# Kernel tuning notes

Measured on AMD Instinct MI355X. Metric: run time of the kernel, lower is better.

Reference implementation:

```python
import jax, jax.numpy as jnp
import numpy as np

S, HID, H, D, G = 2048, 4096, 32, 128, 2   # seq, hidden, heads, head_dim, kv groups
ROT = D // 2                               # rotary applied to first half of head_dim
QKV = HID + 2 * G * D                      # 4608


def setup_inputs() -> dict:
    key = jax.random.key(0)
    k1, k2, k3 = jax.random.split(key, 3)
    sc = 0.02
    return {
        "hidden_states": jax.random.normal(k1, (S, HID), jnp.float32),
        "W_qkv": jax.random.normal(k2, (HID, QKV), jnp.float32) * sc,
        "b_qkv": jnp.zeros((QKV,), jnp.float32),
        "W_dense": jax.random.normal(k3, (HID, HID), jnp.float32) * sc,
    }


def _rope(x, pos):
    # x: [S, n_heads, ROT]; interleaved-pair rotation (ChatGLM2 convention)
    half = ROT // 2
    inv_freq = 10000.0 ** (-jnp.arange(0, ROT, 2, dtype=jnp.float32) / ROT)  # [half]
    theta = pos[:, None] * inv_freq                                          # [S, half]
    cos = jnp.cos(theta)[:, None, :]
    sin = jnp.sin(theta)[:, None, :]
    xp = x.reshape(x.shape[0], x.shape[1], half, 2)
    x0, x1 = xp[..., 0], xp[..., 1]
    out = jnp.stack([x0 * cos - x1 * sin, x1 * cos + x0 * sin], axis=-1)
    return out.reshape(x.shape)


def reference(hidden_states, W_qkv, b_qkv, W_dense):
    qkv = hidden_states @ W_qkv + b_qkv            # [S, QKV]
    q = qkv[:, : H * D].reshape(S, H, D)           # [S, H, D]
    k = qkv[:, H * D : H * D + G * D].reshape(S, G, D)
    v = qkv[:, H * D + G * D :].reshape(S, G, D)

    pos = jnp.arange(S, dtype=jnp.float32)
    q = jnp.concatenate([_rope(q[..., :ROT], pos), q[..., ROT:]], axis=-1)
    k = jnp.concatenate([_rope(k[..., :ROT], pos), k[..., ROT:]], axis=-1)

    gidx = jnp.arange(H) % G                       # head -> kv group (MQA/GQA)
    kh = k[:, gidx, :]                             # [S, H, D]
    vh = v[:, gidx, :]

    scores = jnp.einsum('shd,thd->hst', q, kh) / jnp.sqrt(jnp.float32(D))
    causal = jnp.tril(jnp.ones((S, S), bool))
    scores = jnp.where(causal[None], scores, jnp.float32(-1e9))
    p = jax.nn.softmax(scores, axis=-1)            # [H, S, S]
    ctx = jnp.einsum('hst,thd->shd', p, vh).reshape(S, HID)
    return ctx @ W_dense
```

## Files before the change

kernel.cpp:

```cpp
#include <hip/hip_runtime.h>
#include <hip/hip_bf16.h>

#define S_LEN 2048
#define HIDN  4096
#define NH    32
#define HD    128
#define QKV_N 4608
#define K_OFF 4096
#define V_OFF 4352
#define SCALE 0.08838834764831845f

typedef __attribute__((ext_vector_type(8))) short   short8;
typedef __attribute__((ext_vector_type(4))) float   f32x4;
typedef __attribute__((ext_vector_type(4))) unsigned short ushort4v;
typedef __attribute__((ext_vector_type(8))) unsigned short ushort8;

typedef __attribute__((address_space(1))) const unsigned int GU32;
typedef __attribute__((address_space(3))) unsigned int LU32;

__device__ __forceinline__ void async16(const void* g, void* l) {
  __builtin_amdgcn_global_load_lds((GU32*)g, (LU32*)l, 16, 0, 0);
}

__device__ __forceinline__ unsigned short f2bf(float x) {
  __hip_bfloat16 h = __float2bfloat16(x);
  return *reinterpret_cast<unsigned short*>(&h);
}
__device__ __forceinline__ float bf2f(unsigned short u) {
  __hip_bfloat16 h = *reinterpret_cast<__hip_bfloat16*>(&u);
  return __bfloat162float(h);
}

__global__ void k_cvt_bf16(const float* __restrict__ in, unsigned short* __restrict__ out, int n4) {
  int i = blockIdx.x * 256 + threadIdx.x;
  if (i >= n4) return;
  const float4 v = reinterpret_cast<const float4*>(in)[i];
  ushort4v o = { f2bf(v.x), f2bf(v.y), f2bf(v.z), f2bf(v.w) };
  reinterpret_cast<ushort4v*>(out)[i] = o;
}

__global__ __launch_bounds__(256) void k_transpose_cvt(const float* __restrict__ W,
                                                       unsigned short* __restrict__ WT,
                                                       int K, int N) {
  __shared__ float tl[64][65];
  const int n0 = blockIdx.x * 64, k0 = blockIdx.y * 64;
  const int t = threadIdx.x;
  const int r = t >> 4, c4 = (t & 15) << 2;
#pragma unroll
  for (int p = 0; p < 4; ++p) {
    int krow = p * 16 + r;
    const float4 v = *reinterpret_cast<const float4*>(&W[(size_t)(k0 + krow) * N + n0 + c4]);
    tl[krow][c4 + 0] = v.x; tl[krow][c4 + 1] = v.y;
    tl[krow][c4 + 2] = v.z; tl[krow][c4 + 3] = v.w;
  }
  __syncthreads();
#pragma unroll
  for (int p = 0; p < 4; ++p) {
    int nrow = p * 16 + r;
    ushort4v o = { f2bf(tl[c4 + 0][nrow]), f2bf(tl[c4 + 1][nrow]),
                   f2bf(tl[c4 + 2][nrow]), f2bf(tl[c4 + 3][nrow]) };
    *reinterpret_cast<ushort4v*>(&WT[(size_t)(n0 + nrow) * K + k0 + c4]) = o;
  }
}

template <int BIAS, int OUTBF>
__global__ __launch_bounds__(256, 2) void k_gemm_bt(const unsigned short* __restrict__ A,
                                                    const unsigned short* __restrict__ Bt,
                                                    const float* __restrict__ bias,
                                                    void* __restrict__ Cout,
                                                    int M, int N, int K) {
  __shared__ __align__(16) unsigned char lds[32768];
  const int tid = threadIdx.x;
  const int l = tid & 63, w = tid >> 6;
  const int wr = w >> 1, wc = w & 1;
  const int l16 = l & 15, lh = l >> 4;
  const int nx = N >> 7;
  const int cpx = gridDim.x >> 3;
  const int wg = (blockIdx.x & 7) * cpx + (blockIdx.x >> 3);
  const int m0 = (wg / nx) * 128, n0 = (wg % nx) * 128;
  const size_t rowK = (size_t)K * 2;
  const char* Ab = (const char*)A + (size_t)m0 * rowK;
  const char* Bb = (const char*)Bt + (size_t)n0 * rowK;
  f32x4 acc[4][4] = {};
  const int nkt = K >> 6;
  for (int kt = 0; kt < nkt; ++kt) {
    const int kbyte = kt << 7;
#pragma unroll
    for (int rr = 0; rr < 4; ++rr) {
      int off = rr * 4096 + tid * 16;
      int row = off >> 7;
      int col = (off & 127) ^ ((row & 7) << 4);
      async16(Ab + (size_t)row * rowK + kbyte + col, lds + off);
    }
#pragma unroll
    for (int rr = 0; rr < 4; ++rr) {
      int off = rr * 4096 + tid * 16;
      int row = off >> 7;
      int col = (off & 127) ^ ((row & 7) << 4);
      async16(Bb + (size_t)row * rowK + kbyte + col, lds + 16384 + off);
    }
    __syncthreads();
#pragma unroll
    for (int kk = 0; kk < 2; ++kk) {
      short8 af[4], bfr[4];
#pragma unroll
      for (int m = 0; m < 4; ++m) {
        int arow = wr * 64 + m * 16 + l16;
        int byte = (arow << 7) + kk * 64 + lh * 16;
        byte ^= (arow & 7) << 4;
        af[m] = *reinterpret_cast<const short8*>(lds + byte);
      }
#pragma unroll
      for (int n = 0; n < 4; ++n) {
        int brow = wc * 64 + n * 16 + l16;
        int byte = (brow << 7) + kk * 64 + lh * 16;
        byte ^= (brow & 7) << 4;
        bfr[n] = *reinterpret_cast<const short8*>(lds + 16384 + byte);
      }
#pragma unroll
      for (int m = 0; m < 4; ++m)
#pragma unroll
        for (int n = 0; n < 4; ++n)
          acc[m][n] = __builtin_amdgcn_mfma_f32_16x16x32_bf16(af[m], bfr[n], acc[m][n], 0, 0, 0);
    }
    __syncthreads();
  }
#pragma unroll
  for (int m = 0; m < 4; ++m) {
    int grow = m0 + wr * 64 + m * 16 + lh * 4;
#pragma unroll
    for (int n = 0; n < 4; ++n) {
      int gcol = n0 + wc * 64 + n * 16 + l16;
      float bv = BIAS ? bias[gcol] : 0.f;
      f32x4 v = acc[m][n];
#pragma unroll
      for (int j = 0; j < 4; ++j) {
        float val = v[j] + bv;
        if (OUTBF) ((unsigned short*)Cout)[(size_t)(grow + j) * N + gcol] = f2bf(val);
        else       ((float*)Cout)[(size_t)(grow + j) * N + gcol] = val;
      }
    }
  }
}

__global__ void k_rope(unsigned short* __restrict__ qkv) {
  const int p = blockIdx.x * 64 + threadIdx.x;
  const int s = blockIdx.y;
  const int i = p & 31;
  const int hh = p >> 5;
  const int col = (hh < 32) ? (hh * HD + 2 * i) : (K_OFF + (hh - 32) * HD + 2 * i);
  unsigned int* ptr = (unsigned int*)(qkv + (size_t)s * QKV_N + col);
  unsigned int both = *ptr;
  float x0 = bf2f((unsigned short)(both & 0xffffu));
  float x1 = bf2f((unsigned short)(both >> 16));
  float inv = expf(-0.28782313662425572f * (float)i);
  float theta = (float)s * inv;
  float sn, cs;
  sincosf(theta, &sn, &cs);
  float y0 = x0 * cs - x1 * sn;
  float y1 = x1 * cs + x0 * sn;
  *ptr = (unsigned int)f2bf(y0) | ((unsigned int)f2bf(y1) << 16);
}

__global__ __launch_bounds__(256) void k_transpose_v(const unsigned short* __restrict__ qkv,
                                                     unsigned short* __restrict__ Vt) {
  __shared__ __align__(16) unsigned short tl[64][72];
  const int st = blockIdx.x * 64;
  const int dt = blockIdx.y * 64;
  const int g = blockIdx.z;
  const int t = threadIdx.x;
  const int r = t >> 3;
  const int seg = (t & 7) * 8;
#pragma unroll
  for (int p = 0; p < 2; ++p) {
    int srow = p * 32 + r;
    ushort8 v = *reinterpret_cast<const ushort8*>(
        &qkv[(size_t)(st + srow) * QKV_N + V_OFF + g * HD + dt + seg]);
    *reinterpret_cast<ushort8*>(&tl[srow][seg]) = v;
  }
  __syncthreads();
#pragma unroll
  for (int p = 0; p < 2; ++p) {
    int drow = p * 32 + r;
    ushort8 o;
#pragma unroll
    for (int i = 0; i < 8; ++i) o[i] = tl[seg + i][drow];
    *reinterpret_cast<ushort8*>(&Vt[((size_t)g * HD + dt + drow) * S_LEN + st + seg]) = o;
  }
}

__global__ __launch_bounds__(512) void k_attn(const unsigned short* __restrict__ qkv,
                                              const unsigned short* __restrict__ Vt,
                                              unsigned short* __restrict__ ctx) {
  __shared__ __align__(16) unsigned char lds[81920];
  const int tid = threadIdx.x;
  const int l = tid & 63, w = tid >> 6;
  const int l16 = l & 15, lh = l >> 4;
  const int b = blockIdx.x;
  const int h = b & 31;
  const int g = h & 1;
  const int bt = b >> 5;
  const int tier = (b < 256) ? bt : 23 - bt;
  const int q0 = (15 - tier) * 128;
  const int qw = q0 + w * 16;
  const int nkt = (q0 >> 6) + 2;

  const char* Kbase = (const char*)(qkv + K_OFF + g * HD);
  const char* Vbase = (const char*)(Vt + (size_t)g * HD * S_LEN);

  short8 vones;
#pragma unroll
  for (int e = 0; e < 8; ++e) vones[e] = (short)0x3F80;

  short8 qf[4];
#pragma unroll
  for (int ks = 0; ks < 4; ++ks)
    qf[ks] = *reinterpret_cast<const short8*>(
        qkv + (size_t)(qw + l16) * QKV_N + h * HD + ks * 32 + lh * 8);
  asm volatile("s_waitcnt vmcnt(0)" ::: "memory");

  f32x4 o[8] = {};
  f32x4 lacc = {};
  float m_run = -1e30f;

#pragma unroll
  for (int rr = 0; rr < 2; ++rr) {
    int off = rr * 8192 + tid * 16;
    int row = off >> 8;
    int col = (off & 255) ^ ((row & 7) << 4);
    async16(Kbase + (size_t)row * (QKV_N * 2) + col, lds + off);
  }
#pragma unroll
  for (int rr = 0; rr < 2; ++rr) {
    int off = rr * 8192 + tid * 16;
    int row = off >> 7;
    int col = (off & 127) ^ ((row & 7) << 4);
    async16(Vbase + (size_t)row * (S_LEN * 2) + col, lds + 32768 + off);
  }

  for (int kt = 0; kt < nkt; ++kt) {
    const int k0 = kt << 6;
    if (kt + 1 < nkt) {
      const int bsel = ((kt + 1) & 1) * 16384;
      const int kn = k0 + 64;
      __builtin_amdgcn_sched_barrier(0);
#pragma unroll
      for (int rr = 0; rr < 2; ++rr) {
        int off = rr * 8192 + tid * 16;
        int row = off >> 8;
        int col = (off & 255) ^ ((row & 7) << 4);
        async16(Kbase + (size_t)(kn + row) * (QKV_N * 2) + col, lds + bsel + off);
      }
#pragma unroll
      for (int rr = 0; rr < 2; ++rr) {
        int off = rr * 8192 + tid * 16;
        int row = off >> 7;
        int col = (off & 127) ^ ((row & 7) << 4);
        async16(Vbase + (size_t)row * (S_LEN * 2) + kn * 2 + col, lds + 32768 + bsel + off);
      }
      __builtin_amdgcn_sched_barrier(0);
      asm volatile("s_waitcnt vmcnt(4)" ::: "memory");
    } else {
      asm volatile("s_waitcnt vmcnt(0)" ::: "memory");
    }
    __builtin_amdgcn_s_barrier();
    __builtin_amdgcn_sched_barrier(0);

    const unsigned char* Kl = lds + (kt & 1) * 16384;
    const unsigned char* Vl = lds + 32768 + (kt & 1) * 16384;

    const bool active = (qw + 15 >= k0);
    if (active) {
      f32x4 sf[4] = {};
      __builtin_amdgcn_s_setprio(1);
#pragma unroll
      for (int n = 0; n < 4; ++n) {
        int krow = n * 16 + l16;
        int swz = (krow & 7) << 4;
#pragma unroll
        for (int ks = 0; ks < 4; ++ks) {
          int byte = (krow << 8) + ks * 64 + lh * 16;
          short8 kf = *reinterpret_cast<const short8*>(Kl + (byte ^ swz));
          sf[n] = __builtin_amdgcn_mfma_f32_16x16x32_bf16(qf[ks], kf, sf[n], 0, 0, 0);
        }
      }
      __builtin_amdgcn_s_setprio(0);

      const int qrow0 = qw + lh * 4;
      float tmax = -1e30f;
#pragma unroll
      for (int n = 0; n < 4; ++n) {
        int key = k0 + n * 16 + l16;
#pragma unroll
        for (int j = 0; j < 4; ++j) {
          float v = sf[n][j] * SCALE;
          v = (key <= qrow0 + j) ? v : -1e30f;
          sf[n][j] = v;
          tmax = fmaxf(tmax, v);
        }
      }
#pragma unroll
      for (int d = 1; d < 64; d <<= 1) tmax = fmaxf(tmax, __shfl_xor(tmax, d, 64));
      if (tmax > m_run + 8.f) {
        float fsc = __expf(m_run - tmax);
        m_run = tmax;
#pragma unroll
        for (int n8 = 0; n8 < 8; ++n8) o[n8] *= fsc;
        lacc *= fsc;
      }

      unsigned char* Pb = lds + 65536 + w * 2048;
#pragma unroll
      for (int n = 0; n < 4; ++n)
#pragma unroll
        for (int j = 0; j < 4; ++j) {
          int row = lh * 4 + j;
          int byte = (row << 7) + (n * 16 + l16) * 2;
          byte ^= (row & 7) << 4;
          *(unsigned short*)(Pb + byte) = f2bf(__expf(sf[n][j] - m_run));
        }

      __builtin_amdgcn_s_setprio(1);
#pragma unroll
      for (int kk = 0; kk < 2; ++kk) {
        int pbyte = (l16 << 7) + kk * 64 + lh * 16;
        pbyte ^= (l16 & 7) << 4;
        short8 pa = *reinterpret_cast<const short8*>(Pb + pbyte);
        lacc = __builtin_amdgcn_mfma_f32_16x16x32_bf16(pa, vones, lacc, 0, 0, 0);
#pragma unroll
        for (int n8 = 0; n8 < 8; ++n8) {
          int vrow = n8 * 16 + l16;
          int vbyte = (vrow << 7) + kk * 64 + lh * 16;
          vbyte ^= (vrow & 7) << 4;
          short8 vb = *reinterpret_cast<const short8*>(Vl + vbyte);
          o[n8] = __builtin_amdgcn_mfma_f32_16x16x32_bf16(pa, vb, o[n8], 0, 0, 0);
        }
      }
      __builtin_amdgcn_s_setprio(0);
    }
    __builtin_amdgcn_s_barrier();
  }

#pragma unroll
  for (int n8 = 0; n8 < 8; ++n8) {
    int col = h * HD + n8 * 16 + l16;
#pragma unroll
    for (int j = 0; j < 4; ++j) {
      int row = qw + lh * 4 + j;
      ctx[(size_t)row * HIDN + col] = f2bf(o[n8][j] / lacc[j]);
    }
  }
}

extern "C" void kernel_launch(void* const* d_in, const int* in_sizes, int n_in,
                              void* d_out, int out_size, void* d_ws, size_t ws_size,
                              hipStream_t stream) {
  const float* hidden = (const float*)d_in[0];
  const float* Wqkv = (const float*)d_in[1];
  const float* bqkv = (const float*)d_in[2];
  const float* Wd = (const float*)d_in[3];
  char* ws = (char*)d_ws;
  unsigned short* hid_bf = (unsigned short*)(ws);
  unsigned short* WqkvT  = (unsigned short*)(ws + 16777216);
  unsigned short* WdT    = (unsigned short*)(ws + 54525952);
  unsigned short* qkv    = (unsigned short*)(ws + 88080384);
  unsigned short* Vt     = (unsigned short*)(ws + 106954752);
  unsigned short* ctx    = (unsigned short*)(ws + 108003328);

  k_cvt_bf16<<<8192, 256, 0, stream>>>(hidden, hid_bf, 2097152);
  k_transpose_cvt<<<dim3(72, 64), 256, 0, stream>>>(Wqkv, WqkvT, 4096, 4608);
  k_transpose_cvt<<<dim3(64, 64), 256, 0, stream>>>(Wd, WdT, 4096, 4096);
  k_gemm_bt<1, 1><<<576, 256, 0, stream>>>(hid_bf, WqkvT, bqkv, qkv, 2048, 4608, 4096);
  k_rope<<<dim3(17, 2048), 64, 0, stream>>>(qkv);
  k_transpose_v<<<dim3(32, 2, 2), 256, 0, stream>>>(qkv, Vt);
  k_attn<<<512, 512, 0, stream>>>(qkv, Vt, ctx);
  k_gemm_bt<0, 0><<<512, 256, 0, stream>>>(ctx, WdT, nullptr, d_out, 2048, 4096, 4096);
}
```

Before: 315.8 us.

## Switch attention to 32x32x16 MFMA with 4 waves of 32 query rows

The attention kernel moves from 16x16x32 to 32x32x16 bf16 MFMA tiles, so each wave now owns 32 query rows and blocks shrink from 512 to 256 threads (4 waves). The K/V staging loop is factored into a helper that issues more loads per thread with a wider K swizzle, and the wait count is adjusted to match. The aim is fewer LDS fragment reads per FLOP and better MFMA throughput, at the cost of more accumulator registers per wave and fewer waves per block to hide latency.

```diff
diff --git a/kernel.cpp b/kernel.cpp
--- a/kernel.cpp
+++ b/kernel.cpp
@@ -12,6 +12,7 @@
 
 typedef __attribute__((ext_vector_type(8))) short   short8;
 typedef __attribute__((ext_vector_type(4))) float   f32x4;
+typedef __attribute__((ext_vector_type(16))) float  f32x16;
 typedef __attribute__((ext_vector_type(4))) unsigned short ushort4v;
 typedef __attribute__((ext_vector_type(8))) unsigned short ushort8;
 
@@ -189,20 +190,40 @@
   }
 }
 
-__global__ __launch_bounds__(512) void k_attn(const unsigned short* __restrict__ qkv,
+__device__ __forceinline__ void stage_kv2(const char* Kb, const char* Vb,
+                                          unsigned char* ldsK, unsigned char* ldsV, int tid) {
+  __builtin_amdgcn_sched_barrier(0);
+#pragma unroll
+  for (int rr = 0; rr < 4; ++rr) {
+    int off = rr * 4096 + tid * 16;
+    int row = off >> 8;
+    int col = (off & 255) ^ ((row & 15) << 4);
+    async16(Kb + (size_t)row * (QKV_N * 2) + col, ldsK + off);
+  }
+#pragma unroll
+  for (int rr = 0; rr < 4; ++rr) {
+    int off = rr * 4096 + tid * 16;
+    int row = off >> 7;
+    int col = (off & 127) ^ ((row & 7) << 4);
+    async16(Vb + (size_t)row * (S_LEN * 2) + col, ldsV + off);
+  }
+  __builtin_amdgcn_sched_barrier(0);
+}
+
+__global__ __launch_bounds__(256) void k_attn(const unsigned short* __restrict__ qkv,
                                               const unsigned short* __restrict__ Vt,
                                               unsigned short* __restrict__ ctx) {
   __shared__ __align__(16) unsigned char lds[81920];
   const int tid = threadIdx.x;
   const int l = tid & 63, w = tid >> 6;
-  const int l16 = l & 15, lh = l >> 4;
+  const int l32 = l & 31, hi = l >> 5;
   const int b = blockIdx.x;
   const int h = b & 31;
   const int g = h & 1;
   const int bt = b >> 5;
   const int tier = (b < 256) ? bt : 23 - bt;
   const int q0 = (15 - tier) * 128;
-  const int qw = q0 + w * 16;
+  const int qw = q0 + w * 32;
   const int nkt = (q0 >> 6) + 2;
 
   const char* Kbase = (const char*)(qkv + K_OFF + g * HD);
@@ -212,54 +233,26 @@
 #pragma unroll
   for (int e = 0; e < 8; ++e) vones[e] = (short)0x3F80;
 
-  short8 qf[4];
-#pragma unroll
-  for (int ks = 0; ks < 4; ++ks)
+  short8 qf[8];
+#pragma unroll
+  for (int ks = 0; ks < 8; ++ks)
     qf[ks] = *reinterpret_cast<const short8*>(
-        qkv + (size_t)(qw + l16) * QKV_N + h * HD + ks * 32 + lh * 8);
+        qkv + (size_t)(qw + l32) * QKV_N + h * HD + ks * 16 + hi * 8);
   asm volatile("s_waitcnt vmcnt(0)" ::: "memory");
 
-  f32x4 o[8] = {};
-  f32x4 lacc = {};
+  f32x16 o[4] = {};
+  f32x16 lacc = {};
   float m_run = -1e30f;
 
-#pragma unroll
-  for (int rr = 0; rr < 2; ++rr) {
-    int off = rr * 8192 + tid * 16;
-    int row = off >> 8;
-    int col = (off & 255) ^ ((row & 7) << 4);
-    async16(Kbase + (size_t)row * (QKV_N * 2) + col, lds + off);
-  }
-#pragma unroll
-  for (int rr = 0; rr < 2; ++rr) {
-    int off = rr * 8192 + tid * 16;
-    int row = off >> 7;
-    int col = (off & 127) ^ ((row & 7) << 4);
-    async16(Vbase + (size_t)row * (S_LEN * 2) + col, lds + 32768 + off);
-  }
+  stage_kv2(Kbase, Vbase, lds, lds + 32768, tid);
 
   for (int kt = 0; kt < nkt; ++kt) {
     const int k0 = kt << 6;
     if (kt + 1 < nkt) {
       const int bsel = ((kt + 1) & 1) * 16384;
-      const int kn = k0 + 64;
-      __builtin_amdgcn_sched_barrier(0);
-#pragma unroll
-      for (int rr = 0; rr < 2; ++rr) {
-        int off = rr * 8192 + tid * 16;
-        int row = off >> 8;
-        int col = (off & 255) ^ ((row & 7) << 4);
-        async16(Kbase + (size_t)(kn + row) * (QKV_N * 2) + col, lds + bsel + off);
-      }
-#pragma unroll
-      for (int rr = 0; rr < 2; ++rr) {
-        int off = rr * 8192 + tid * 16;
-        int row = off >> 7;
-        int col = (off & 127) ^ ((row & 7) << 4);
-        async16(Vbase + (size_t)row * (S_LEN * 2) + kn * 2 + col, lds + 32768 + bsel + off);
-      }
-      __builtin_amdgcn_sched_barrier(0);
-      asm volatile("s_waitcnt vmcnt(4)" ::: "memory");
+      stage_kv2(Kbase + (size_t)(k0 + 64) * (QKV_N * 2), Vbase + (size_t)(k0 + 64) * 2,
+                lds + bsel, lds + 32768 + bsel, tid);
+      asm volatile("s_waitcnt vmcnt(8)" ::: "memory");
     } else {
       asm volatile("s_waitcnt vmcnt(0)" ::: "memory");
     }
@@ -269,33 +262,32 @@
     const unsigned char* Kl = lds + (kt & 1) * 16384;
     const unsigned char* Vl = lds + 32768 + (kt & 1) * 16384;
 
-    const bool active = (qw + 15 >= k0);
+    const bool active = (qw + 31 >= k0);
     if (active) {
-      f32x4 sf[4] = {};
+      f32x16 sf[2] = {};
       __builtin_amdgcn_s_setprio(1);
 #pragma unroll
-      for (int n = 0; n < 4; ++n) {
-        int krow = n * 16 + l16;
-        int swz = (krow & 7) << 4;
-#pragma unroll
-        for (int ks = 0; ks < 4; ++ks) {
-          int byte = (krow << 8) + ks * 64 + lh * 16;
-          short8 kf = *reinterpret_cast<const short8*>(Kl + (byte ^ swz));
-          sf[n] = __builtin_amdgcn_mfma_f32_16x16x32_bf16(qf[ks], kf, sf[n], 0, 0, 0);
+      for (int ks = 0; ks < 8; ++ks)
+#pragma unroll
+        for (int kb = 0; kb < 2; ++kb) {
+          int krow = kb * 32 + l32;
+          int byte = krow * 256 + ks * 32 + hi * 16;
+          byte ^= (krow & 15) << 4;
+          short8 kf = *reinterpret_cast<const short8*>(Kl + byte);
+          sf[kb] = __builtin_amdgcn_mfma_f32_32x32x16_bf16(qf[ks], kf, sf[kb], 0, 0, 0);
         }
-      }
       __builtin_amdgcn_s_setprio(0);
 
-      const int qrow0 = qw + lh * 4;
       float tmax = -1e30f;
 #pragma unroll
-      for (int n = 0; n < 4; ++n) {
-        int key = k0 + n * 16 + l16;
-#pragma unroll
-        for (int j = 0; j < 4; ++j) {
-          float v = sf[n][j] * SCALE;
-          v = (key <= qrow0 + j) ? v : -1e30f;
-          sf[n][j] = v;
+      for (int kb = 0; kb < 2; ++kb) {
+        int key = k0 + kb * 32 + l32;
+#pragma unroll
+        for (int r = 0; r < 16; ++r) {
+          int qrow = qw + (r & 3) + 8 * (r >> 2) + 4 * hi;
+          float v = sf[kb][r] * SCALE;
+          v = (key <= qrow) ? v : -1e30f;
+          sf[kb][r] = v;
           tmax = fmaxf(tmax, v);
         }
       }
@@ -305,35 +297,35 @@
         float fsc = __expf(m_run - tmax);
         m_run = tmax;
 #pragma unroll
-        for (int n8 = 0; n8 < 8; ++n8) o[n8] *= fsc;
+        for (int nf = 0; nf < 4; ++nf) o[nf] *= fsc;
         lacc *= fsc;
       }
 
-      unsigned char* Pb = lds + 65536 + w * 2048;
-#pragma unroll
-      for (int n = 0; n < 4; ++n)
-#pragma unroll
-        for (int j = 0; j < 4; ++j) {
-          int row = lh * 4 + j;
-          int byte = (row << 7) + (n * 16 + l16) * 2;
+      unsigned char* Pw = lds + 65536 + w * 4096;
+#pragma unroll
+      for (int kb = 0; kb < 2; ++kb)
+#pragma unroll
+        for (int r = 0; r < 16; ++r) {
+          int row = (r & 3) + 8 * (r >> 2) + 4 * hi;
+          int byte = row * 128 + (kb * 32 + l32) * 2;
           byte ^= (row & 7) << 4;
-          *(unsigned short*)(Pb + byte) = f2bf(__expf(sf[n][j] - m_run));
+          *(unsigned short*)(Pw + byte) = f2bf(__expf(sf[kb][r] - m_run));
         }
 
       __builtin_amdgcn_s_setprio(1);
 #pragma unroll
-      for (int kk = 0; kk < 2; ++kk) {
-        int pbyte = (l16 << 7) + kk * 64 + lh * 16;
-        pbyte ^= (l16 & 7) << 4;
-        short8 pa = *reinterpret_cast<const short8*>(Pb + pbyte);
-        lacc = __builtin_amdgcn_mfma_f32_16x16x32_bf16(pa, vones, lacc, 0, 0, 0);
-#pragma unroll
-        for (int n8 = 0; n8 < 8; ++n8) {
-          int vrow = n8 * 16 + l16;
-          int vbyte = (vrow << 7) + kk * 64 + lh * 16;
-          vbyte ^= (vrow & 7) << 4;
+      for (int ks4 = 0; ks4 < 4; ++ks4) {
+        int pbyte = l32 * 128 + (ks4 * 16 + hi * 8) * 2;
+        pbyte ^= (l32 & 7) << 4;
+        short8 pa = *reinterpret_cast<const short8*>(Pw + pbyte);
+        lacc = __builtin_amdgcn_mfma_f32_32x32x16_bf16(pa, vones, lacc, 0, 0, 0);
+#pragma unroll
+        for (int nf = 0; nf < 4; ++nf) {
+          int drow = nf * 32 + l32;
+          int vbyte = drow * 128 + ks4 * 32 + hi * 16;
+          vbyte ^= (drow & 7) << 4;
           short8 vb = *reinterpret_cast<const short8*>(Vl + vbyte);
-          o[n8] = __builtin_amdgcn_mfma_f32_16x16x32_bf16(pa, vb, o[n8], 0, 0, 0);
+          o[nf] = __builtin_amdgcn_mfma_f32_32x32x16_bf16(pa, vb, o[nf], 0, 0, 0);
         }
       }
       __builtin_amdgcn_s_setprio(0);
@@ -342,12 +334,12 @@
   }
 
 #pragma unroll
-  for (int n8 = 0; n8 < 8; ++n8) {
-    int col = h * HD + n8 * 16 + l16;
-#pragma unroll
-    for (int j = 0; j < 4; ++j) {
-      int row = qw + lh * 4 + j;
-      ctx[(size_t)row * HIDN + col] = f2bf(o[n8][j] / lacc[j]);
+  for (int nf = 0; nf < 4; ++nf) {
+    int col = h * HD + nf * 32 + l32;
+#pragma unroll
+    for (int r = 0; r < 16; ++r) {
+      int row = qw + (r & 3) + 8 * (r >> 2) + 4 * hi;
+      ctx[(size_t)row * HIDN + col] = f2bf(o[nf][r] / lacc[r]);
     }
   }
 }
@@ -373,6 +365,6 @@
   k_gemm_bt<1, 1><<<576, 256, 0, stream>>>(hid_bf, WqkvT, bqkv, qkv, 2048, 4608, 4096);
   k_rope<<<dim3(17, 2048), 64, 0, stream>>>(qkv);
   k_transpose_v<<<dim3(32, 2, 2), 256, 0, stream>>>(qkv, Vt);
-  k_attn<<<512, 512, 0, stream>>>(qkv, Vt, ctx);
+  k_attn<<<512, 256, 0, stream>>>(qkv, Vt, ctx);
   k_gemm_bt<0, 0><<<512, 256, 0, stream>>>(ctx, WdT, nullptr, d_out, 2048, 4096, 4096);
 }
```

New measurement: 344.6 us. +9.1%, slower.

## Process 32 query rows per wave in attention to reuse K/V fragments

Applied to the files above, without the earlier changes.

The attention kernel now runs 4 waves of 256 threads per block instead of 8, and each wave handles two 16-row query tiles. Each K and V fragment read from LDS feeds two MFMAs, which halves LDS reads per unit of compute. K/V staging is split into more, smaller loads per thread, and the K swizzle is widened to 16 rows. In exchange, accumulator registers double and there are fewer waves to hide latency. Causal skipping also becomes coarser, so some masked work is wasted.

```diff
diff --git a/kernel.cpp b/kernel.cpp
--- a/kernel.cpp
+++ b/kernel.cpp
@@ -189,7 +189,27 @@
   }
 }
 
-__global__ __launch_bounds__(512) void k_attn(const unsigned short* __restrict__ qkv,
+__device__ __forceinline__ void stage_kv2(const char* Kb, const char* Vb,
+                                          unsigned char* ldsK, unsigned char* ldsV, int tid) {
+  __builtin_amdgcn_sched_barrier(0);
+#pragma unroll
+  for (int rr = 0; rr < 4; ++rr) {
+    int off = rr * 4096 + tid * 16;
+    int row = off >> 8;
+    int col = (off & 255) ^ ((row & 15) << 4);
+    async16(Kb + (size_t)row * (QKV_N * 2) + col, ldsK + off);
+  }
+#pragma unroll
+  for (int rr = 0; rr < 4; ++rr) {
+    int off = rr * 4096 + tid * 16;
+    int row = off >> 7;
+    int col = (off & 127) ^ ((row & 7) << 4);
+    async16(Vb + (size_t)row * (S_LEN * 2) + col, ldsV + off);
+  }
+  __builtin_amdgcn_sched_barrier(0);
+}
+
+__global__ __launch_bounds__(256) void k_attn(const unsigned short* __restrict__ qkv,
                                               const unsigned short* __restrict__ Vt,
                                               unsigned short* __restrict__ ctx) {
   __shared__ __align__(16) unsigned char lds[81920];
@@ -202,7 +222,7 @@
   const int bt = b >> 5;
   const int tier = (b < 256) ? bt : 23 - bt;
   const int q0 = (15 - tier) * 128;
-  const int qw = q0 + w * 16;
+  const int qw = q0 + w * 32;
   const int nkt = (q0 >> 6) + 2;
 
   const char* Kbase = (const char*)(qkv + K_OFF + g * HD);
@@ -212,54 +232,28 @@
 #pragma unroll
   for (int e = 0; e < 8; ++e) vones[e] = (short)0x3F80;
 
-  short8 qf[4];
-#pragma unroll
-  for (int ks = 0; ks < 4; ++ks)
-    qf[ks] = *reinterpret_cast<const short8*>(
-        qkv + (size_t)(qw + l16) * QKV_N + h * HD + ks * 32 + lh * 8);
+  short8 qf[2][4];
+#pragma unroll
+  for (int m = 0; m < 2; ++m)
+#pragma unroll
+    for (int ks = 0; ks < 4; ++ks)
+      qf[m][ks] = *reinterpret_cast<const short8*>(
+          qkv + (size_t)(qw + m * 16 + l16) * QKV_N + h * HD + ks * 32 + lh * 8);
   asm volatile("s_waitcnt vmcnt(0)" ::: "memory");
 
-  f32x4 o[8] = {};
-  f32x4 lacc = {};
+  f32x4 o[2][8] = {};
+  f32x4 lacc[2] = {};
   float m_run = -1e30f;
 
-#pragma unroll
-  for (int rr = 0; rr < 2; ++rr) {
-    int off = rr * 8192 + tid * 16;
-    int row = off >> 8;
-    int col = (off & 255) ^ ((row & 7) << 4);
-    async16(Kbase + (size_t)row * (QKV_N * 2) + col, lds + off);
-  }
-#pragma unroll
-  for (int rr = 0; rr < 2; ++rr) {
-    int off = rr * 8192 + tid * 16;
-    int row = off >> 7;
-    int col = (off & 127) ^ ((row & 7) << 4);
-    async16(Vbase + (size_t)row * (S_LEN * 2) + col, lds + 32768 + off);
-  }
+  stage_kv2(Kbase, Vbase, lds, lds + 32768, tid);
 
   for (int kt = 0; kt < nkt; ++kt) {
     const int k0 = kt << 6;
     if (kt + 1 < nkt) {
       const int bsel = ((kt + 1) & 1) * 16384;
-      const int kn = k0 + 64;
-      __builtin_amdgcn_sched_barrier(0);
-#pragma unroll
-      for (int rr = 0; rr < 2; ++rr) {
-        int off = rr * 8192 + tid * 16;
-        int row = off >> 8;
-        int col = (off & 255) ^ ((row & 7) << 4);
-        async16(Kbase + (size_t)(kn + row) * (QKV_N * 2) + col, lds + bsel + off);
-      }
-#pragma unroll
-      for (int rr = 0; rr < 2; ++rr) {
-        int off = rr * 8192 + tid * 16;
-        int row = off >> 7;
-        int col = (off & 127) ^ ((row & 7) << 4);
-        async16(Vbase + (size_t)row * (S_LEN * 2) + kn * 2 + col, lds + 32768 + bsel + off);
-      }
-      __builtin_amdgcn_sched_barrier(0);
-      asm volatile("s_waitcnt vmcnt(4)" ::: "memory");
+      stage_kv2(Kbase + (size_t)(k0 + 64) * (QKV_N * 2), Vbase + (size_t)(k0 + 64) * 2,
+                lds + bsel, lds + 32768 + bsel, tid);
+      asm volatile("s_waitcnt vmcnt(8)" ::: "memory");
     } else {
       asm volatile("s_waitcnt vmcnt(0)" ::: "memory");
     }
@@ -269,34 +263,39 @@
     const unsigned char* Kl = lds + (kt & 1) * 16384;
     const unsigned char* Vl = lds + 32768 + (kt & 1) * 16384;
 
-    const bool active = (qw + 15 >= k0);
+    const bool active = (qw + 31 >= k0);
     if (active) {
-      f32x4 sf[4] = {};
+      f32x4 sf[2][4] = {};
       __builtin_amdgcn_s_setprio(1);
 #pragma unroll
       for (int n = 0; n < 4; ++n) {
         int krow = n * 16 + l16;
-        int swz = (krow & 7) << 4;
+        int swz = (krow & 15) << 4;
 #pragma unroll
         for (int ks = 0; ks < 4; ++ks) {
           int byte = (krow << 8) + ks * 64 + lh * 16;
           short8 kf = *reinterpret_cast<const short8*>(Kl + (byte ^ swz));
-          sf[n] = __builtin_amdgcn_mfma_f32_16x16x32_bf16(qf[ks], kf, sf[n], 0, 0, 0);
+#pragma unroll
+          for (int m = 0; m < 2; ++m)
+            sf[m][n] = __builtin_amdgcn_mfma_f32_16x16x32_bf16(qf[m][ks], kf, sf[m][n], 0, 0, 0);
         }
       }
       __builtin_amdgcn_s_setprio(0);
 
-      const int qrow0 = qw + lh * 4;
       float tmax = -1e30f;
 #pragma unroll
-      for (int n = 0; n < 4; ++n) {
-        int key = k0 + n * 16 + l16;
-#pragma unroll
-        for (int j = 0; j < 4; ++j) {
-          float v = sf[n][j] * SCALE;
-          v = (key <= qrow0 + j) ? v : -1e30f;
-          sf[n][j] = v;
-          tmax = fmaxf(tmax, v);
+      for (int m = 0; m < 2; ++m) {
+        const int qrow0 = qw + m * 16 + lh * 4;
+#pragma unroll
+        for (int n = 0; n < 4; ++n) {
+          int key = k0 + n * 16 + l16;
+#pragma unroll
+          for (int j = 0; j < 4; ++j) {
+            float v = sf[m][n][j] * SCALE;
+            v = (key <= qrow0 + j) ? v : -1e30f;
+            sf[m][n][j] = v;
+            tmax = fmaxf(tmax, v);
+          }
         }
       }
 #pragma unroll
@@ -305,35 +304,47 @@
         float fsc = __expf(m_run - tmax);
         m_run = tmax;
 #pragma unroll
-        for (int n8 = 0; n8 < 8; ++n8) o[n8] *= fsc;
-        lacc *= fsc;
-      }
-
-      unsigned char* Pb = lds + 65536 + w * 2048;
-#pragma unroll
-      for (int n = 0; n < 4; ++n)
-#pragma unroll
-        for (int j = 0; j < 4; ++j) {
-          int row = lh * 4 + j;
-          int byte = (row << 7) + (n * 16 + l16) * 2;
-          byte ^= (row & 7) << 4;
-          *(unsigned short*)(Pb + byte) = f2bf(__expf(sf[n][j] - m_run));
-        }
+        for (int m = 0; m < 2; ++m) {
+#pragma unroll
+          for (int n8 = 0; n8 < 8; ++n8) o[m][n8] *= fsc;
+          lacc[m] *= fsc;
+        }
+      }
+
+      unsigned char* Pw = lds + 65536 + w * 4096;
+#pragma unroll
+      for (int m = 0; m < 2; ++m)
+#pragma unroll
+        for (int n = 0; n < 4; ++n)
+#pragma unroll
+          for (int j = 0; j < 4; ++j) {
+            int row = m * 16 + lh * 4 + j;
+            int byte = (row << 7) + (n * 16 + l16) * 2;
+            byte ^= (row & 7) << 4;
+            *(unsigned short*)(Pw + byte) = f2bf(__expf(sf[m][n][j] - m_run));
+          }
 
       __builtin_amdgcn_s_setprio(1);
 #pragma unroll
       for (int kk = 0; kk < 2; ++kk) {
-        int pbyte = (l16 << 7) + kk * 64 + lh * 16;
-        pbyte ^= (l16 & 7) << 4;
-        short8 pa = *reinterpret_cast<const short8*>(Pb + pbyte);
-        lacc = __builtin_amdgcn_mfma_f32_16x16x32_bf16(pa, vones, lacc, 0, 0, 0);
+        short8 pa[2];
+#pragma unroll
+        for (int m = 0; m < 2; ++m) {
+          int prow = m * 16 + l16;
+          int pbyte = (prow << 7) + kk * 64 + lh * 16;
+          pbyte ^= (prow & 7) << 4;
+          pa[m] = *reinterpret_cast<const short8*>(Pw + pbyte);
+          lacc[m] = __builtin_amdgcn_mfma_f32_16x16x32_bf16(pa[m], vones, lacc[m], 0, 0, 0);
+        }
 #pragma unroll
         for (int n8 = 0; n8 < 8; ++n8) {
           int vrow = n8 * 16 + l16;
           int vbyte = (vrow << 7) + kk * 64 + lh * 16;
           vbyte ^= (vrow & 7) << 4;
           short8 vb = *reinterpret_cast<const short8*>(Vl + vbyte);
-          o[n8] = __builtin_amdgcn_mfma_f32_16x16x32_bf16(pa, vb, o[n8], 0, 0, 0);
+#pragma unroll
+          for (int m = 0; m < 2; ++m)
+            o[m][n8] = __builtin_amdgcn_mfma_f32_16x16x32_bf16(pa[m], vb, o[m][n8], 0, 0, 0);
         }
       }
       __builtin_amdgcn_s_setprio(0);
@@ -342,14 +353,16 @@
   }
 
 #pragma unroll
-  for (int n8 = 0; n8 < 8; ++n8) {
-    int col = h * HD + n8 * 16 + l16;
-#pragma unroll
-    for (int j = 0; j < 4; ++j) {
-      int row = qw + lh * 4 + j;
-      ctx[(size_t)row * HIDN + col] = f2bf(o[n8][j] / lacc[j]);
-    }
-  }
+  for (int m = 0; m < 2; ++m)
+#pragma unroll
+    for (int n8 = 0; n8 < 8; ++n8) {
+      int col = h * HD + n8 * 16 + l16;
+#pragma unroll
+      for (int j = 0; j < 4; ++j) {
+        int row = qw + m * 16 + lh * 4 + j;
+        ctx[(size_t)row * HIDN + col] = f2bf(o[m][n8][j] / lacc[m][j]);
+      }
+    }
 }
 
 extern "C" void kernel_launch(void* const* d_in, const int* in_sizes, int n_in,
@@ -373,6 +386,6 @@
   k_gemm_bt<1, 1><<<576, 256, 0, stream>>>(hid_bf, WqkvT, bqkv, qkv, 2048, 4608, 4096);
   k_rope<<<dim3(17, 2048), 64, 0, stream>>>(qkv);
   k_transpose_v<<<dim3(32, 2, 2), 256, 0, stream>>>(qkv, Vt);
-  k_attn<<<512, 512, 0, stream>>>(qkv, Vt, ctx);
+  k_attn<<<512, 256, 0, stream>>>(qkv, Vt, ctx);
   k_gemm_bt<0, 0><<<512, 256, 0, stream>>>(ctx, WdT, nullptr, d_out, 2048, 4096, 4096);
 }
```

Measured after the change: 347.8 us. 10.1% more time.
